# Optimization experiments

Measured on AMD Instinct MI355X. Metric: run time of the kernel, lower is better.

Reference implementation:

```python
import jax, jax.numpy as jnp
import numpy as np

N = 8192
H = 128  # node_size == hidden_size (required by a1/a2 applied to Wh)
NEG_BIG = -9e15


def setup_inputs() -> dict:
    key = jax.random.key(0)
    k1, k2, k3, k4, k5, k6, k7 = jax.random.split(key, 7)
    node_fea = jax.random.normal(k1, (N, H), dtype=jnp.float32)
    edge_fea = jax.random.normal(k2, (N, N, 1), dtype=jnp.float32)
    adj = jax.random.randint(k3, (N, N), 0, 2, dtype=jnp.int32)
    # learned params (nn.Linear: y = x @ W.T + b)
    s = 1.0 / np.sqrt(H)
    W_w = jax.random.uniform(k4, (H, H), dtype=jnp.float32, minval=-s, maxval=s)
    W_b = jax.random.uniform(k5, (H,), dtype=jnp.float32, minval=-s, maxval=s)
    a1_w = jax.random.uniform(k6, (1, H), dtype=jnp.float32, minval=-s, maxval=s)
    a2_w = jax.random.uniform(k7, (1, H), dtype=jnp.float32, minval=-s, maxval=s)
    return {"node_fea": node_fea, "edge_fea": edge_fea, "adj": adj,
            "W_w": W_w, "W_b": W_b, "a1_w": a1_w, "a2_w": a2_w}


def reference(node_fea, edge_fea, adj, W_w, W_b, a1_w, a2_w):
    # GAT_layer.forward with is_mix_attention=False (the shape-consistent path).
    Wh = node_fea @ W_w.T + W_b                      # [N, H]
    Whi = Wh @ a1_w.T                                # [N, 1]
    Whj = Wh @ a2_w.T                                # [N, 1]
    e = jax.nn.leaky_relu(Whi + Whj.T, 0.2)          # [N, N] broadcast add
    e = jnp.where(adj > 0, e, NEG_BIG)               # masked fill
    attention = jax.nn.softmax(e, axis=-1)           # F.softmax on 2D -> dim=1
    # dropout omitted (eval-mode / deterministic reference)
    node_fea_new = attention @ Wh + Wh               # [N, H]
    return node_fea_new, edge_fea                    # edge_fea passes through
```

## Files before the change

### kernel.cpp

```cpp
#include <hip/hip_runtime.h>

#define NN 8192
#define HH 128
#define JSPLIT 16
#define SEG (NN / JSPLIT)
#define CHUNKS (SEG / 32)

typedef float f32x4 __attribute__((ext_vector_type(4)));
typedef short bf16x8 __attribute__((ext_vector_type(8)));
typedef unsigned short u16;
typedef unsigned int u32;

__device__ __forceinline__ u16 f2bf(float f) {
    u32 u = __float_as_uint(f);
    u32 r = (u + 0x7FFFu + ((u >> 16) & 1u)) >> 16;
    return (u16)r;
}

__global__ __launch_bounds__(256) void k_wh(const float* __restrict__ X,
                                            const float* __restrict__ Ww,
                                            const float* __restrict__ Wb,
                                            float* __restrict__ Wh) {
    __shared__ float xT[128][38];
    __shared__ float wT[128][68];
    const int tid = threadIdx.x;
    const int r0 = blockIdx.x * 32;

#pragma unroll
    for (int p = 0; p < 4; ++p) {
        int idx = p * 256 + tid;
        int r = idx >> 5, kq = idx & 31;
        float4 v = *(const float4*)&X[(r0 + r) * HH + kq * 4];
        xT[kq * 4 + 0][r] = v.x; xT[kq * 4 + 1][r] = v.y;
        xT[kq * 4 + 2][r] = v.z; xT[kq * 4 + 3][r] = v.w;
    }
    const int rg = tid >> 4;
    const int cg = tid & 15;

    for (int ch = 0; ch < 2; ++ch) {
        __syncthreads();
#pragma unroll
        for (int p = 0; p < 8; ++p) {
            int idx = p * 256 + tid;
            int cc = idx >> 5, kq = idx & 31;
            float4 v = *(const float4*)&Ww[(ch * 64 + cc) * HH + kq * 4];
            wT[kq * 4 + 0][cc] = v.x; wT[kq * 4 + 1][cc] = v.y;
            wT[kq * 4 + 2][cc] = v.z; wT[kq * 4 + 3][cc] = v.w;
        }
        __syncthreads();
        float acc0[4] = {0.f, 0.f, 0.f, 0.f};
        float acc1[4] = {0.f, 0.f, 0.f, 0.f};
#pragma unroll 4
        for (int k = 0; k < 128; ++k) {
            float2 xv = *(const float2*)&xT[k][rg * 2];
            f32x4 wv = *(const f32x4*)&wT[k][cg * 4];
#pragma unroll
            for (int j = 0; j < 4; ++j) {
                acc0[j] += xv.x * wv[j];
                acc1[j] += xv.y * wv[j];
            }
        }
        f32x4 bv = *(const f32x4*)&Wb[ch * 64 + cg * 4];
        f32x4 o0 = {acc0[0] + bv[0], acc0[1] + bv[1], acc0[2] + bv[2], acc0[3] + bv[3]};
        f32x4 o1 = {acc1[0] + bv[0], acc1[1] + bv[1], acc1[2] + bv[2], acc1[3] + bv[3]};
        *(f32x4*)&Wh[(r0 + rg * 2 + 0) * HH + ch * 64 + cg * 4] = o0;
        *(f32x4*)&Wh[(r0 + rg * 2 + 1) * HH + ch * 64 + cg * 4] = o1;
    }
}

__global__ __launch_bounds__(256) void k_tr(const float* __restrict__ Wh,
                                            const float* __restrict__ a1,
                                            const float* __restrict__ a2,
                                            u16* __restrict__ WhT,
                                            float* __restrict__ Whi,
                                            float* __restrict__ Whj) {
    __shared__ u16 tb[128][72];
    const int tid = threadIdx.x;
    const int r0 = blockIdx.x * 64;
    const int c4 = tid & 31;
    const int rloc = tid >> 5;
    f32x4 a1v = *(const f32x4*)&a1[c4 * 4];
    f32x4 a2v = *(const f32x4*)&a2[c4 * 4];
#pragma unroll
    for (int p = 0; p < 8; ++p) {
        int r = p * 8 + rloc;
        f32x4 v = *(const f32x4*)&Wh[(r0 + r) * HH + c4 * 4];
        tb[c4 * 4 + 0][r] = f2bf(v[0]); tb[c4 * 4 + 1][r] = f2bf(v[1]);
        tb[c4 * 4 + 2][r] = f2bf(v[2]); tb[c4 * 4 + 3][r] = f2bf(v[3]);
        float pi = v[0] * a1v[0] + v[1] * a1v[1] + v[2] * a1v[2] + v[3] * a1v[3];
        float pj = v[0] * a2v[0] + v[1] * a2v[1] + v[2] * a2v[2] + v[3] * a2v[3];
#pragma unroll
        for (int s = 16; s >= 1; s >>= 1) {
            pi += __shfl_xor(pi, s);
            pj += __shfl_xor(pj, s);
        }
        if (c4 == 0) { Whi[r0 + r] = pi; Whj[r0 + r] = pj; }
    }
    __syncthreads();
    const int c = tid >> 1, half = tid & 1;
#pragma unroll
    for (int q = 0; q < 4; ++q) {
        int4 v = *(const int4*)&tb[c][half * 32 + q * 8];
        *(int4*)&WhT[c * NN + r0 + half * 32 + q * 8] = v;
    }
}

#define PEL(whiv, av, wjv, zz, oute)                                      \
    {                                                                     \
        float s_ = (whiv) + (wjv);                                        \
        s_ = s_ > 0.f ? s_ : 0.2f * s_;                                   \
        float w_ = ((av) > 0) ? __expf(s_) : 0.f;                         \
        zz += w_;                                                         \
        oute = (short)f2bf(w_);                                           \
    }

__global__ __launch_bounds__(256) void k_attn(const int* __restrict__ adj,
                                              const u16* __restrict__ WhT,
                                              const float* __restrict__ Whi,
                                              const float* __restrict__ Whj,
                                              float* __restrict__ accP,
                                              float* __restrict__ Zp) {
    const int tid = threadIdx.x;
    const int wave = tid >> 6, lane = tid & 63;
    const int m = lane & 15, g = lane >> 4;
    const int kbase = g * 8;
    const int r0 = blockIdx.x * 128 + wave * 32;
    const int j0b = blockIdx.y * SEG;
    const int row0 = r0 + m, row1 = r0 + 16 + m;
    const float whi0 = Whi[row0], whi1 = Whi[row1];
    const int* arow0 = adj + row0 * NN + j0b;
    const int* arow1 = adj + row1 * NN + j0b;
    const float* wjp = Whj + j0b;
    const u16* bbase = WhT + m * NN + j0b;

    f32x4 acc[2][8];
#pragma unroll
    for (int a = 0; a < 2; ++a)
#pragma unroll
        for (int b = 0; b < 8; ++b) acc[a][b] = (f32x4){0.f, 0.f, 0.f, 0.f};
    float z0 = 0.f, z1 = 0.f;

    for (int cch = 0; cch < CHUNKS; ++cch) {
        const int jo = cch * 32 + kbase;
        f32x4 wj0 = *(const f32x4*)&wjp[jo];
        f32x4 wj1 = *(const f32x4*)&wjp[jo + 4];
        int4 a00 = *(const int4*)&arow0[jo];
        int4 a01 = *(const int4*)&arow0[jo + 4];
        int4 a10 = *(const int4*)&arow1[jo];
        int4 a11 = *(const int4*)&arow1[jo + 4];
        bf16x8 pa0, pa1;
        PEL(whi0, a00.x, wj0[0], z0, pa0[0]); PEL(whi0, a00.y, wj0[1], z0, pa0[1]);
        PEL(whi0, a00.z, wj0[2], z0, pa0[2]); PEL(whi0, a00.w, wj0[3], z0, pa0[3]);
        PEL(whi0, a01.x, wj1[0], z0, pa0[4]); PEL(whi0, a01.y, wj1[1], z0, pa0[5]);
        PEL(whi0, a01.z, wj1[2], z0, pa0[6]); PEL(whi0, a01.w, wj1[3], z0, pa0[7]);
        PEL(whi1, a10.x, wj0[0], z1, pa1[0]); PEL(whi1, a10.y, wj0[1], z1, pa1[1]);
        PEL(whi1, a10.z, wj0[2], z1, pa1[2]); PEL(whi1, a10.w, wj0[3], z1, pa1[3]);
        PEL(whi1, a11.x, wj1[0], z1, pa1[4]); PEL(whi1, a11.y, wj1[1], z1, pa1[5]);
        PEL(whi1, a11.z, wj1[2], z1, pa1[6]); PEL(whi1, a11.w, wj1[3], z1, pa1[7]);

        const u16* bp = bbase + jo;
#pragma unroll
        for (int ct = 0; ct < 8; ++ct) {
            bf16x8 bfr = *(const bf16x8*)(bp + ct * 16 * NN);
            acc[0][ct] = __builtin_amdgcn_mfma_f32_16x16x32_bf16(pa0, bfr, acc[0][ct], 0, 0, 0);
            acc[1][ct] = __builtin_amdgcn_mfma_f32_16x16x32_bf16(pa1, bfr, acc[1][ct], 0, 0, 0);
        }
    }

    z0 += __shfl_xor(z0, 16); z0 += __shfl_xor(z0, 32);
    z1 += __shfl_xor(z1, 16); z1 += __shfl_xor(z1, 32);
    if (lane < 16) {
        Zp[blockIdx.y * NN + r0 + lane] = z0;
        Zp[blockIdx.y * NN + r0 + 16 + lane] = z1;
    }
    const long base = (long)blockIdx.y * NN * HH;
#pragma unroll
    for (int it = 0; it < 2; ++it)
#pragma unroll
        for (int ct = 0; ct < 8; ++ct)
#pragma unroll
            for (int reg = 0; reg < 4; ++reg) {
                int row = r0 + it * 16 + g * 4 + reg;
                accP[base + row * HH + ct * 16 + m] = acc[it][ct][reg];
            }
}

__global__ __launch_bounds__(256) void k_red(const float* __restrict__ accP,
                                             const float* __restrict__ Zp,
                                             const float* __restrict__ Wh,
                                             float* __restrict__ out) {
    const int gidx = blockIdx.x * 256 + threadIdx.x;
    const int i = gidx >> 5;
    const int c4 = (gidx & 31) * 4;
    f32x4 s = {0.f, 0.f, 0.f, 0.f};
    float z = 0.f;
#pragma unroll
    for (int sg = 0; sg < JSPLIT; ++sg) {
        s += *(const f32x4*)&accP[sg * (NN * HH) + i * HH + c4];
        z += Zp[sg * NN + i];
    }
    f32x4 whv = *(const f32x4*)&Wh[i * HH + c4];
    f32x4 o = s * (1.f / z) + whv;
    *(f32x4*)&out[i * HH + c4] = o;
}

__global__ __launch_bounds__(256) void k_copy(const f32x4* __restrict__ src,
                                              f32x4* __restrict__ dst, int n4) {
    int idx = blockIdx.x * 256 + threadIdx.x;
    const int stride = gridDim.x * 256;
    for (; idx < n4; idx += stride) dst[idx] = src[idx];
}

extern "C" void kernel_launch(void* const* d_in, const int* in_sizes, int n_in,
                              void* d_out, int out_size, void* d_ws, size_t ws_size,
                              hipStream_t stream) {
    const float* node = (const float*)d_in[0];
    const float* edge = (const float*)d_in[1];
    const int*   adj  = (const int*)d_in[2];
    const float* Ww   = (const float*)d_in[3];
    const float* Wb   = (const float*)d_in[4];
    const float* a1   = (const float*)d_in[5];
    const float* a2   = (const float*)d_in[6];
    float* out = (float*)d_out;

    const size_t OFF_WH  = 0;
    const size_t OFF_WHI = (size_t)4 * 1024 * 1024;
    const size_t OFF_WHJ = OFF_WHI + 32 * 1024;
    const size_t OFF_ZP  = OFF_WHJ + 32 * 1024;
    const size_t OFF_AP  = OFF_ZP + 512 * 1024;
    const size_t OFF_WHT = OFF_AP + (size_t)64 * 1024 * 1024;
    const size_t NEED    = OFF_WHT + (size_t)2 * 1024 * 1024;

    char* scratch = (ws_size >= NEED) ? (char*)d_ws
                                      : (char*)d_out + (size_t)NN * HH * 4;
    float* Wh   = (float*)(scratch + OFF_WH);
    float* Whi  = (float*)(scratch + OFF_WHI);
    float* Whj  = (float*)(scratch + OFF_WHJ);
    float* Zp   = (float*)(scratch + OFF_ZP);
    float* accP = (float*)(scratch + OFF_AP);
    u16*   WhT  = (u16*)(scratch + OFF_WHT);

    k_wh<<<dim3(256), 256, 0, stream>>>(node, Ww, Wb, Wh);
    k_tr<<<dim3(128), 256, 0, stream>>>(Wh, a1, a2, WhT, Whi, Whj);
    k_attn<<<dim3(64, JSPLIT), 256, 0, stream>>>(adj, WhT, Whi, Whj, accP, Zp);
    k_red<<<dim3(1024), 256, 0, stream>>>(accP, Zp, Wh, out);
    k_copy<<<dim3(4096), 256, 0, stream>>>((const f32x4*)edge,
                                           (f32x4*)(out + (size_t)NN * HH),
                                           NN * NN / 4);
}
```

Baseline: 691.8 us.

## Fuse projection with transpose, overlap edge copy with attention, halve split

Merges the Wh projection and the bf16 transpose/attention-logit kernel into one pre-kernel, so Wh is not re-read. The edge_fea passthrough copy now runs in extra blocks of the attention kernel, so the memory-bound copy overlaps the adjacency streaming and MFMA work. JSPLIT drops from 16 to 8, which halves partial-accumulator traffic but leaves fewer attention blocks. The main loop also software-prefetches the next chunk's adjacency and Whj values. The copy blocks and attention blocks compete for the same HBM bandwidth.

```diff
diff --git a/kernel.cpp b/kernel.cpp
--- a/kernel.cpp
+++ b/kernel.cpp
@@ -2,9 +2,12 @@
 
 #define NN 8192
 #define HH 128
-#define JSPLIT 16
+#define JSPLIT 8
 #define SEG (NN / JSPLIT)
 #define CHUNKS (SEG / 32)
+#define COPY_BLOCKS 256
+#define ATTN_BLOCKS (64 * JSPLIT)
+#define COPY_PER_BLOCK ((NN * NN / 4) / COPY_BLOCKS)
 
 typedef float f32x4 __attribute__((ext_vector_type(4)));
 typedef short bf16x8 __attribute__((ext_vector_type(8)));
@@ -17,12 +20,18 @@
     return (u16)r;
 }
 
-__global__ __launch_bounds__(256) void k_wh(const float* __restrict__ X,
-                                            const float* __restrict__ Ww,
-                                            const float* __restrict__ Wb,
-                                            float* __restrict__ Wh) {
+__global__ __launch_bounds__(256) void k_pre(const float* __restrict__ X,
+                                             const float* __restrict__ Ww,
+                                             const float* __restrict__ Wb,
+                                             const float* __restrict__ a1,
+                                             const float* __restrict__ a2,
+                                             float* __restrict__ Wh,
+                                             u16* __restrict__ WhT,
+                                             float* __restrict__ Whi,
+                                             float* __restrict__ Whj) {
     __shared__ float xT[128][38];
     __shared__ float wT[128][68];
+    __shared__ u16 tb[128][40];
     const int tid = threadIdx.x;
     const int r0 = blockIdx.x * 32;
 
@@ -36,6 +45,7 @@
     }
     const int rg = tid >> 4;
     const int cg = tid & 15;
+    float pi0 = 0.f, pi1 = 0.f, pj0 = 0.f, pj1 = 0.f;
 
     for (int ch = 0; ch < 2; ++ch) {
         __syncthreads();
@@ -60,48 +70,39 @@
                 acc1[j] += xv.y * wv[j];
             }
         }
-        f32x4 bv = *(const f32x4*)&Wb[ch * 64 + cg * 4];
+        f32x4 bv  = *(const f32x4*)&Wb[ch * 64 + cg * 4];
+        f32x4 a1v = *(const f32x4*)&a1[ch * 64 + cg * 4];
+        f32x4 a2v = *(const f32x4*)&a2[ch * 64 + cg * 4];
         f32x4 o0 = {acc0[0] + bv[0], acc0[1] + bv[1], acc0[2] + bv[2], acc0[3] + bv[3]};
         f32x4 o1 = {acc1[0] + bv[0], acc1[1] + bv[1], acc1[2] + bv[2], acc1[3] + bv[3]};
         *(f32x4*)&Wh[(r0 + rg * 2 + 0) * HH + ch * 64 + cg * 4] = o0;
         *(f32x4*)&Wh[(r0 + rg * 2 + 1) * HH + ch * 64 + cg * 4] = o1;
-    }
-}
-
-__global__ __launch_bounds__(256) void k_tr(const float* __restrict__ Wh,
-                                            const float* __restrict__ a1,
-                                            const float* __restrict__ a2,
-                                            u16* __restrict__ WhT,
-                                            float* __restrict__ Whi,
-                                            float* __restrict__ Whj) {
-    __shared__ u16 tb[128][72];
-    const int tid = threadIdx.x;
-    const int r0 = blockIdx.x * 64;
-    const int c4 = tid & 31;
-    const int rloc = tid >> 5;
-    f32x4 a1v = *(const f32x4*)&a1[c4 * 4];
-    f32x4 a2v = *(const f32x4*)&a2[c4 * 4];
-#pragma unroll
-    for (int p = 0; p < 8; ++p) {
-        int r = p * 8 + rloc;
-        f32x4 v = *(const f32x4*)&Wh[(r0 + r) * HH + c4 * 4];
-        tb[c4 * 4 + 0][r] = f2bf(v[0]); tb[c4 * 4 + 1][r] = f2bf(v[1]);
-        tb[c4 * 4 + 2][r] = f2bf(v[2]); tb[c4 * 4 + 3][r] = f2bf(v[3]);
-        float pi = v[0] * a1v[0] + v[1] * a1v[1] + v[2] * a1v[2] + v[3] * a1v[3];
-        float pj = v[0] * a2v[0] + v[1] * a2v[1] + v[2] * a2v[2] + v[3] * a2v[3];
-#pragma unroll
-        for (int s = 16; s >= 1; s >>= 1) {
-            pi += __shfl_xor(pi, s);
-            pj += __shfl_xor(pj, s);
-        }
-        if (c4 == 0) { Whi[r0 + r] = pi; Whj[r0 + r] = pj; }
+#pragma unroll
+        for (int j = 0; j < 4; ++j) {
+            tb[ch * 64 + cg * 4 + j][rg * 2 + 0] = f2bf(o0[j]);
+            tb[ch * 64 + cg * 4 + j][rg * 2 + 1] = f2bf(o1[j]);
+        }
+#pragma unroll
+        for (int j = 0; j < 4; ++j) {
+            pi0 += o0[j] * a1v[j]; pj0 += o0[j] * a2v[j];
+            pi1 += o1[j] * a1v[j]; pj1 += o1[j] * a2v[j];
+        }
+    }
+#pragma unroll
+    for (int s = 8; s >= 1; s >>= 1) {
+        pi0 += __shfl_xor(pi0, s); pj0 += __shfl_xor(pj0, s);
+        pi1 += __shfl_xor(pi1, s); pj1 += __shfl_xor(pj1, s);
+    }
+    if (cg == 0) {
+        Whi[r0 + rg * 2 + 0] = pi0; Whj[r0 + rg * 2 + 0] = pj0;
+        Whi[r0 + rg * 2 + 1] = pi1; Whj[r0 + rg * 2 + 1] = pj1;
     }
     __syncthreads();
-    const int c = tid >> 1, half = tid & 1;
-#pragma unroll
-    for (int q = 0; q < 4; ++q) {
-        int4 v = *(const int4*)&tb[c][half * 32 + q * 8];
-        *(int4*)&WhT[c * NN + r0 + half * 32 + q * 8] = v;
+    const int c = tid >> 1, h = tid & 1;
+#pragma unroll
+    for (int q = 0; q < 2; ++q) {
+        int4 v = *(const int4*)&tb[c][h * 16 + q * 8];
+        *(int4*)&WhT[(size_t)c * NN + r0 + h * 16 + q * 8] = v;
     }
 }
 
@@ -114,24 +115,38 @@
         oute = (short)f2bf(w_);                                           \
     }
 
-__global__ __launch_bounds__(256) void k_attn(const int* __restrict__ adj,
+__global__ __launch_bounds__(256) void k_main(const int* __restrict__ adj,
                                               const u16* __restrict__ WhT,
                                               const float* __restrict__ Whi,
                                               const float* __restrict__ Whj,
+                                              const f32x4* __restrict__ edge,
+                                              f32x4* __restrict__ edst,
                                               float* __restrict__ accP,
-                                              float* __restrict__ Zp) {
+                                              float* __restrict__ Zp,
+                                              int fused_copy) {
+    const int bid = blockIdx.x;
+    if (bid < COPY_BLOCKS) {
+        if (!fused_copy) return;
+        const int base = bid * COPY_PER_BLOCK + threadIdx.x;
+#pragma unroll 8
+        for (int k = 0; k < COPY_PER_BLOCK / 256; ++k)
+            edst[base + k * 256] = edge[base + k * 256];
+        return;
+    }
+    const int ab = bid - COPY_BLOCKS;
+    const int rb = ab & 63, seg = ab >> 6;
     const int tid = threadIdx.x;
     const int wave = tid >> 6, lane = tid & 63;
     const int m = lane & 15, g = lane >> 4;
     const int kbase = g * 8;
-    const int r0 = blockIdx.x * 128 + wave * 32;
-    const int j0b = blockIdx.y * SEG;
+    const int r0 = rb * 128 + wave * 32;
+    const int j0b = seg * SEG;
     const int row0 = r0 + m, row1 = r0 + 16 + m;
     const float whi0 = Whi[row0], whi1 = Whi[row1];
-    const int* arow0 = adj + row0 * NN + j0b;
-    const int* arow1 = adj + row1 * NN + j0b;
+    const int* arow0 = adj + (size_t)row0 * NN + j0b;
+    const int* arow1 = adj + (size_t)row1 * NN + j0b;
     const float* wjp = Whj + j0b;
-    const u16* bbase = WhT + m * NN + j0b;
+    const u16* bbase = WhT + (size_t)m * NN + j0b;
 
     f32x4 acc[2][8];
 #pragma unroll
@@ -140,40 +155,59 @@
         for (int b = 0; b < 8; ++b) acc[a][b] = (f32x4){0.f, 0.f, 0.f, 0.f};
     float z0 = 0.f, z1 = 0.f;
 
+    int jo = kbase;
+    f32x4 cw0 = *(const f32x4*)&wjp[jo];
+    f32x4 cw1 = *(const f32x4*)&wjp[jo + 4];
+    int4 c00 = *(const int4*)&arow0[jo];
+    int4 c01 = *(const int4*)&arow0[jo + 4];
+    int4 c10 = *(const int4*)&arow1[jo];
+    int4 c11 = *(const int4*)&arow1[jo + 4];
+
     for (int cch = 0; cch < CHUNKS; ++cch) {
-        const int jo = cch * 32 + kbase;
-        f32x4 wj0 = *(const f32x4*)&wjp[jo];
-        f32x4 wj1 = *(const f32x4*)&wjp[jo + 4];
-        int4 a00 = *(const int4*)&arow0[jo];
-        int4 a01 = *(const int4*)&arow0[jo + 4];
-        int4 a10 = *(const int4*)&arow1[jo];
-        int4 a11 = *(const int4*)&arow1[jo + 4];
+        const int jn = (cch + 1 < CHUNKS ? cch + 1 : cch) * 32 + kbase;
+        f32x4 nw0 = *(const f32x4*)&wjp[jn];
+        f32x4 nw1 = *(const f32x4*)&wjp[jn + 4];
+        int4 n00 = *(const int4*)&arow0[jn];
+        int4 n01 = *(const int4*)&arow0[jn + 4];
+        int4 n10 = *(const int4*)&arow1[jn];
+        int4 n11 = *(const int4*)&arow1[jn + 4];
+
         bf16x8 pa0, pa1;
-        PEL(whi0, a00.x, wj0[0], z0, pa0[0]); PEL(whi0, a00.y, wj0[1], z0, pa0[1]);
-        PEL(whi0, a00.z, wj0[2], z0, pa0[2]); PEL(whi0, a00.w, wj0[3], z0, pa0[3]);
-        PEL(whi0, a01.x, wj1[0], z0, pa0[4]); PEL(whi0, a01.y, wj1[1], z0, pa0[5]);
-        PEL(whi0, a01.z, wj1[2], z0, pa0[6]); PEL(whi0, a01.w, wj1[3], z0, pa0[7]);
-        PEL(whi1, a10.x, wj0[0], z1, pa1[0]); PEL(whi1, a10.y, wj0[1], z1, pa1[1]);
-        PEL(whi1, a10.z, wj0[2], z1, pa1[2]); PEL(whi1, a10.w, wj0[3], z1, pa1[3]);
-        PEL(whi1, a11.x, wj1[0], z1, pa1[4]); PEL(whi1, a11.y, wj1[1], z1, pa1[5]);
-        PEL(whi1, a11.z, wj1[2], z1, pa1[6]); PEL(whi1, a11.w, wj1[3], z1, pa1[7]);
-
-        const u16* bp = bbase + jo;
-#pragma unroll
-        for (int ct = 0; ct < 8; ++ct) {
-            bf16x8 bfr = *(const bf16x8*)(bp + ct * 16 * NN);
-            acc[0][ct] = __builtin_amdgcn_mfma_f32_16x16x32_bf16(pa0, bfr, acc[0][ct], 0, 0, 0);
-            acc[1][ct] = __builtin_amdgcn_mfma_f32_16x16x32_bf16(pa1, bfr, acc[1][ct], 0, 0, 0);
-        }
+        PEL(whi0, c00.x, cw0[0], z0, pa0[0]); PEL(whi0, c00.y, cw0[1], z0, pa0[1]);
+        PEL(whi0, c00.z, cw0[2], z0, pa0[2]); PEL(whi0, c00.w, cw0[3], z0, pa0[3]);
+        PEL(whi0, c01.x, cw1[0], z0, pa0[4]); PEL(whi0, c01.y, cw1[1], z0, pa0[5]);
+        PEL(whi0, c01.z, cw1[2], z0, pa0[6]); PEL(whi0, c01.w, cw1[3], z0, pa0[7]);
+        PEL(whi1, c10.x, cw0[0], z1, pa1[0]); PEL(whi1, c10.y, cw0[1], z1, pa1[1]);
+        PEL(whi1, c10.z, cw0[2], z1, pa1[2]); PEL(whi1, c10.w, cw0[3], z1, pa1[3]);
+        PEL(whi1, c11.x, cw1[0], z1, pa1[4]); PEL(whi1, c11.y, cw1[1], z1, pa1[5]);
+        PEL(whi1, c11.z, cw1[2], z1, pa1[6]); PEL(whi1, c11.w, cw1[3], z1, pa1[7]);
+
+        const u16* bp = bbase + cch * 32 + kbase;
+#pragma unroll
+        for (int hh = 0; hh < 2; ++hh) {
+            bf16x8 bfr[4];
+#pragma unroll
+            for (int t = 0; t < 4; ++t)
+                bfr[t] = *(const bf16x8*)(bp + (size_t)(hh * 4 + t) * 16 * NN);
+#pragma unroll
+            for (int t = 0; t < 4; ++t) {
+                acc[0][hh * 4 + t] = __builtin_amdgcn_mfma_f32_16x16x32_bf16(
+                    pa0, bfr[t], acc[0][hh * 4 + t], 0, 0, 0);
+                acc[1][hh * 4 + t] = __builtin_amdgcn_mfma_f32_16x16x32_bf16(
+                    pa1, bfr[t], acc[1][hh * 4 + t], 0, 0, 0);
+            }
+        }
+        cw0 = nw0; cw1 = nw1;
+        c00 = n00; c01 = n01; c10 = n10; c11 = n11;
     }
 
     z0 += __shfl_xor(z0, 16); z0 += __shfl_xor(z0, 32);
     z1 += __shfl_xor(z1, 16); z1 += __shfl_xor(z1, 32);
     if (lane < 16) {
-        Zp[blockIdx.y * NN + r0 + lane] = z0;
-        Zp[blockIdx.y * NN + r0 + 16 + lane] = z1;
-    }
-    const long base = (long)blockIdx.y * NN * HH;
+        Zp[(size_t)seg * NN + r0 + lane] = z0;
+        Zp[(size_t)seg * NN + r0 + 16 + lane] = z1;
+    }
+    const size_t base = (size_t)seg * NN * HH;
 #pragma unroll
     for (int it = 0; it < 2; ++it)
 #pragma unroll
@@ -181,7 +215,7 @@
 #pragma unroll
             for (int reg = 0; reg < 4; ++reg) {
                 int row = r0 + it * 16 + g * 4 + reg;
-                accP[base + row * HH + ct * 16 + m] = acc[it][ct][reg];
+                accP[base + (size_t)row * HH + ct * 16 + m] = acc[it][ct][reg];
             }
 }
 
@@ -196,12 +230,12 @@
     float z = 0.f;
 #pragma unroll
     for (int sg = 0; sg < JSPLIT; ++sg) {
-        s += *(const f32x4*)&accP[sg * (NN * HH) + i * HH + c4];
-        z += Zp[sg * NN + i];
-    }
-    f32x4 whv = *(const f32x4*)&Wh[i * HH + c4];
+        s += *(const f32x4*)&accP[(size_t)sg * (NN * HH) + (size_t)i * HH + c4];
+        z += Zp[(size_t)sg * NN + i];
+    }
+    f32x4 whv = *(const f32x4*)&Wh[(size_t)i * HH + c4];
     f32x4 o = s * (1.f / z) + whv;
-    *(f32x4*)&out[i * HH + c4] = o;
+    *(f32x4*)&out[(size_t)i * HH + c4] = o;
 }
 
 __global__ __launch_bounds__(256) void k_copy(const f32x4* __restrict__ src,
@@ -228,23 +262,23 @@
     const size_t OFF_WHJ = OFF_WHI + 32 * 1024;
     const size_t OFF_ZP  = OFF_WHJ + 32 * 1024;
     const size_t OFF_AP  = OFF_ZP + 512 * 1024;
-    const size_t OFF_WHT = OFF_AP + (size_t)64 * 1024 * 1024;
+    const size_t OFF_WHT = OFF_AP + (size_t)JSPLIT * NN * HH * 4;
     const size_t NEED    = OFF_WHT + (size_t)2 * 1024 * 1024;
 
-    char* scratch = (ws_size >= NEED) ? (char*)d_ws
-                                      : (char*)d_out + (size_t)NN * HH * 4;
+    const bool fits = (ws_size >= NEED);
+    char* scratch = fits ? (char*)d_ws : (char*)d_out + (size_t)NN * HH * 4;
     float* Wh   = (float*)(scratch + OFF_WH);
     float* Whi  = (float*)(scratch + OFF_WHI);
     float* Whj  = (float*)(scratch + OFF_WHJ);
     float* Zp   = (float*)(scratch + OFF_ZP);
     float* accP = (float*)(scratch + OFF_AP);
     u16*   WhT  = (u16*)(scratch + OFF_WHT);
-
-    k_wh<<<dim3(256), 256, 0, stream>>>(node, Ww, Wb, Wh);
-    k_tr<<<dim3(128), 256, 0, stream>>>(Wh, a1, a2, WhT, Whi, Whj);
-    k_attn<<<dim3(64, JSPLIT), 256, 0, stream>>>(adj, WhT, Whi, Whj, accP, Zp);
+    f32x4* edst = (f32x4*)(out + (size_t)NN * HH);
+
+    k_pre<<<dim3(256), 256, 0, stream>>>(node, Ww, Wb, a1, a2, Wh, WhT, Whi, Whj);
+    k_main<<<dim3(COPY_BLOCKS + ATTN_BLOCKS), 256, 0, stream>>>(
+        adj, WhT, Whi, Whj, (const f32x4*)edge, edst, accP, Zp, fits ? 1 : 0);
     k_red<<<dim3(1024), 256, 0, stream>>>(accP, Zp, Wh, out);
-    k_copy<<<dim3(4096), 256, 0, stream>>>((const f32x4*)edge,
-                                           (f32x4*)(out + (size_t)NN * HH),
-                                           NN * NN / 4);
-}
+    if (!fits)
+        k_copy<<<dim3(4096), 256, 0, stream>>>((const f32x4*)edge, edst, NN * NN / 4);
+}
```

Result: faster. 665.3 us (-3.8%).
